# Performance work log

Measured on AMD Instinct MI355X. Metric: run time of the kernel, lower is better.

Reference implementation:

```python
import jax, jax.numpy as jnp
import numpy as np

B, N1, N2 = 4, 2048, 8192
F_IN, F_OUT = 256, 256
K = 3          # PyG knn_interpolate default
BN_EPS = 1e-5


def linear_bn(x, W, b, gamma, beta):
    # Linear + BatchNorm1d (training mode: batch stats over B*N per feature)
    h = jnp.einsum('bni,io->bno', x, W) + b
    mean = h.mean(axis=(0, 1))
    var = h.var(axis=(0, 1))
    xhat = (h - mean) * jax.lax.rsqrt(var + BN_EPS)
    return gamma * xhat + beta


def knn_interpolate(f1, p1, p2):
    # f1: [N1,F], p1: [N1,3], p2: [N2,3] -> [N2,F]
    d2 = jnp.sum((p2[:, None, :] - p1[None, :, :]) ** 2, axis=-1)  # [N2,N1]
    neg_d2, idx = jax.lax.top_k(-d2, K)                            # k smallest
    w = 1.0 / jnp.maximum(-neg_d2, 1e-16)                          # [N2,K]
    fk = f1[idx]                                                   # [N2,K,F]
    return jnp.sum(w[..., None] * fk, axis=1) / jnp.sum(w, axis=1, keepdims=True)


def setup_inputs() -> dict:
    key = jax.random.key(0)
    ks = jax.random.split(key, 10)
    return {
        'features_1': jax.random.normal(ks[0], (B, N1, F_IN), jnp.float32),
        'positions_1': jax.random.uniform(ks[1], (B, N1, 3), jnp.float32),
        'batch_1': jnp.repeat(jnp.arange(B, dtype=jnp.int64), N1),
        'features_2': jax.random.normal(ks[2], (B, N2, F_IN), jnp.float32),
        'positions_2': jax.random.uniform(ks[3], (B, N2, 3), jnp.float32),
        'batch_2': jnp.repeat(jnp.arange(B, dtype=jnp.int64), N2),
        'W1': jax.random.normal(ks[4], (F_IN, F_OUT), jnp.float32) * (1.0 / np.sqrt(F_IN)),
        'b1': jax.random.normal(ks[5], (F_OUT,), jnp.float32) * 0.02,
        'gamma1': jnp.ones((F_OUT,), jnp.float32),
        'beta1': jnp.zeros((F_OUT,), jnp.float32),
        'W2': jax.random.normal(ks[6], (F_IN, F_OUT), jnp.float32) * (1.0 / np.sqrt(F_IN)),
        'b2': jax.random.normal(ks[7], (F_OUT,), jnp.float32) * 0.02,
        'gamma2': jnp.ones((F_OUT,), jnp.float32),
        'beta2': jnp.zeros((F_OUT,), jnp.float32),
    }


def reference(features_1, positions_1, batch_1, features_2, positions_2, batch_2,
              W1, b1, gamma1, beta1, W2, b2, gamma2, beta2):
    f1 = linear_bn(features_1, W1, b1, gamma1, beta1)          # [B,N1,F_OUT]
    f2 = linear_bn(features_2, W2, b2, gamma2, beta2)          # [B,N2,F_OUT]
    # batch structure is regular [B,N]: knn restricted within batch == vmap over B
    interp = jax.vmap(knn_interpolate)(f1, positions_1, positions_2)  # [B,N2,F_OUT]
    return (interp + f2, positions_2, batch_2)
```

## Files before the change

kernel.cpp:

```cpp
#include <hip/hip_runtime.h>
#include <math.h>

#define BATCH   4
#define N1      2048
#define N2      8192
#define F       256
#define NTOT1   (BATCH * N1)
#define NTOT2   (BATCH * N2)
#define BN_EPS  1e-5f

#define GR      6
#define NC      216
#define NCP     (NC + 1)
#define GH      (1.0f / 6.0f)

typedef __attribute__((ext_vector_type(8))) short bf16x8;
typedef __attribute__((ext_vector_type(4))) float f32x4;

__device__ __forceinline__ unsigned short f2bf(float f) {
    unsigned u = __float_as_uint(f);
    unsigned r = (u + 0x7fffu + ((u >> 16) & 1u)) >> 16;
    return (unsigned short)r;
}
__device__ __forceinline__ float bflo(unsigned u) {
    return __uint_as_float(u << 16);
}
__device__ __forceinline__ float bfhi(unsigned u) {
    return __uint_as_float(u & 0xffff0000u);
}
__device__ __forceinline__ void async16(const void* g, void* l) {
    __builtin_amdgcn_global_load_lds(
        (const __attribute__((address_space(1))) unsigned int*)g,
        (__attribute__((address_space(3))) unsigned int*)l, 16, 0, 0);
}

__device__ __forceinline__ void ins3m(float d, int j,
                                      float& d0, float& d1, float& d2,
                                      int& j0, int& j1, int& j2) {
    const bool c0 = d < d0;
    const bool c1 = d < d1;
    const bool c2 = d < d2;
    const float nd1 = __builtin_amdgcn_fmed3f(d, d0, d1);
    const float nd2 = __builtin_amdgcn_fmed3f(d, d1, d2);
    d0 = fminf(d, d0);
    d1 = nd1;
    d2 = nd2;
    j2 = c1 ? j1 : (c2 ? j : j2);
    j1 = c0 ? j0 : (c1 ? j : j1);
    j0 = c0 ? j  : j0;
}

__device__ __forceinline__ int clamp6(int c) { return c < 0 ? 0 : (c > 5 ? 5 : c); }
__device__ __forceinline__ int cell_of(float x, float y, float z) {
    const int cx = clamp6((int)(x * 6.0f));
    const int cy = clamp6((int)(y * 6.0f));
    const int cz = clamp6((int)(z * 6.0f));
    return (cz * 6 + cy) * 6 + cx;
}

__global__ __launch_bounds__(256) void prep_kernel(const float4* __restrict__ f1,
                                                   const float4* __restrict__ f2,
                                                   const float* __restrict__ W1,
                                                   const float* __restrict__ W2,
                                                   const float* __restrict__ p1,
                                                   const float* __restrict__ p2,
                                                   ushort4* __restrict__ Xb1,
                                                   ushort4* __restrict__ Xb2,
                                                   unsigned short* __restrict__ Wt1,
                                                   unsigned short* __restrict__ Wt2,
                                                   float* __restrict__ sums,
                                                   float4* __restrict__ gridPts,
                                                   int* __restrict__ cellStart,
                                                   int* __restrict__ qSorted,
                                                   int* __restrict__ qCellStart) {
    const int bx = blockIdx.x;
    const int t  = threadIdx.x;

    if (bx < 8192) {
        const int i = bx * 256 + t;
        const float4 v = f2[i];
        ushort4 o;
        o.x = f2bf(v.x); o.y = f2bf(v.y); o.z = f2bf(v.z); o.w = f2bf(v.w);
        Xb2[i] = o;
    } else if (bx < 10240) {
        const int i = (bx - 8192) * 256 + t;
        const float4 v = f1[i];
        ushort4 o;
        o.x = f2bf(v.x); o.y = f2bf(v.y); o.z = f2bf(v.z); o.w = f2bf(v.w);
        Xb1[i] = o;
    } else if (bx < 10272) {
        __shared__ float tile[64][65];
        const int bb = bx - 10240;
        const bool second = bb >= 16;
        const int bl = second ? bb - 16 : bb;
        const float* W = second ? W2 : W1;
        unsigned short* Wt = second ? Wt2 : Wt1;
        const int gx0 = (bl & 3) * 64;
        const int gy0 = (bl >> 2) * 64;
        const int tx = t & 63;
        const int ty = t >> 6;
        #pragma unroll
        for (int j = 0; j < 16; ++j) {
            const int row = ty * 16 + j;
            tile[row][tx] = W[(size_t)(gy0 + row) * 256 + gx0 + tx];
        }
        __syncthreads();
        #pragma unroll
        for (int j = 0; j < 16; ++j) {
            const int row = ty * 16 + j;
            Wt[(size_t)(gx0 + row) * 256 + gy0 + tx] = f2bf(tile[tx][row]);
        }
    } else if (bx == 10272) {
        #pragma unroll
        for (int i = 0; i < 4; ++i) sums[t + 256 * i] = 0.0f;
    } else if (bx < 10277) {
        __shared__ int cnt[NC];
        __shared__ int ofs[NCP];
        const int b = bx - 10273;
        if (t < NC) cnt[t] = 0;
        __syncthreads();
        int   myc[8];
        float mx[8], my[8], mz[8];
        #pragma unroll
        for (int r = 0; r < 8; ++r) {
            const int i = r * 256 + t;
            const size_t base = (size_t)(b * N1 + i) * 3;
            mx[r] = p1[base]; my[r] = p1[base + 1]; mz[r] = p1[base + 2];
            myc[r] = cell_of(mx[r], my[r], mz[r]);
            atomicAdd(&cnt[myc[r]], 1);
        }
        __syncthreads();
        if (t <= NC) ofs[t] = (t == 0) ? 0 : cnt[t - 1];
        __syncthreads();
        for (int dd = 1; dd < NCP; dd <<= 1) {
            int v = 0;
            if (t <= NC && t >= dd) v = ofs[t - dd];
            __syncthreads();
            if (t <= NC && t >= dd) ofs[t] += v;
            __syncthreads();
        }
        if (t < NC) cnt[t] = ofs[t];
        __syncthreads();
        #pragma unroll
        for (int r = 0; r < 8; ++r) {
            const int i = r * 256 + t;
            const int pos = atomicAdd(&cnt[myc[r]], 1);
            float4 rec;
            rec.x = mx[r]; rec.y = my[r]; rec.z = mz[r];
            rec.w = __int_as_float(i);
            gridPts[(size_t)b * N1 + pos] = rec;
        }
        if (t <= NC) cellStart[b * NCP + t] = ofs[t];
    } else {
        __shared__ int cnt[NC];
        __shared__ int ofs[NCP];
        const int b = bx - 10277;
        if (t < NC) cnt[t] = 0;
        __syncthreads();
        for (int r = 0; r < 32; ++r) {
            const int i = r * 256 + t;
            const size_t base = (size_t)(b * N2 + i) * 3;
            const int c = cell_of(p2[base], p2[base + 1], p2[base + 2]);
            atomicAdd(&cnt[c], 1);
        }
        __syncthreads();
        if (t <= NC) ofs[t] = (t == 0) ? 0 : cnt[t - 1];
        __syncthreads();
        for (int dd = 1; dd < NCP; dd <<= 1) {
            int v = 0;
            if (t <= NC && t >= dd) v = ofs[t - dd];
            __syncthreads();
            if (t <= NC && t >= dd) ofs[t] += v;
            __syncthreads();
        }
        if (t < NC) cnt[t] = ofs[t];
        __syncthreads();
        for (int r = 0; r < 32; ++r) {
            const int i = r * 256 + t;
            const size_t base = (size_t)(b * N2 + i) * 3;
            const int c = cell_of(p2[base], p2[base + 1], p2[base + 2]);
            const int pos = atomicAdd(&cnt[c], 1);
            qSorted[(size_t)b * N2 + pos] = b * N2 + i;
        }
        if (t <= NC) qCellStart[b * NCP + t] = ofs[t];
    }
}

__global__ __launch_bounds__(256) void gemm_mfma_kernel(const unsigned short* __restrict__ Xb1,
                                                        const unsigned short* __restrict__ Xb2,
                                                        const unsigned short* __restrict__ Wt1,
                                                        const unsigned short* __restrict__ Wt2,
                                                        const float* __restrict__ b1,
                                                        const float* __restrict__ b2,
                                                        unsigned short* __restrict__ h1b,
                                                        unsigned short* __restrict__ h2b,
                                                        float* __restrict__ sums) {
    __shared__ unsigned short As[128 * 32];
    __shared__ unsigned short Bs[128 * 32];

    const int bx   = blockIdx.x;
    const bool g2  = bx >= 64;
    const unsigned short* Xb = g2 ? Xb2 : Xb1;
    const unsigned short* Wt = g2 ? Wt2 : Wt1;
    const float* bias        = g2 ? b2 : b1;
    unsigned short* Hb       = g2 ? h2b : h1b;
    float* sum               = sums + (g2 ? 512 : 0);
    float* sumsq             = sum + 256;
    const int row0 = (g2 ? bx - 64 : bx) * 128;
    const int n0   = blockIdx.y * 128;

    const int t    = threadIdx.x;
    const int wave = t >> 6;
    const int lane = t & 63;
    const int wm   = (wave & 1) * 64;
    const int wn   = (wave >> 1) * 64;
    const int ml   = lane & 15;
    const int q    = lane >> 4;

    f32x4 acc[4][4] = {};

    for (int kt = 0; kt < 256; kt += 32) {
        #pragma unroll
        for (int r = 0; r < 2; ++r) {
            const int e   = r * 2048 + t * 8;
            const int row = e >> 5;
            const int kk  = e & 31;
            async16(Xb + (size_t)(row0 + row) * 256 + kt + kk, (unsigned short*)As + e);
            async16(Wt + (size_t)(n0 + row) * 256 + kt + kk, (unsigned short*)Bs + e);
        }
        __syncthreads();

        bf16x8 af[4], bfr[4];
        #pragma unroll
        for (int mt = 0; mt < 4; ++mt)
            af[mt] = *(const bf16x8*)&As[(wm + mt * 16 + ml) * 32 + q * 8];
        #pragma unroll
        for (int nt = 0; nt < 4; ++nt)
            bfr[nt] = *(const bf16x8*)&Bs[(wn + nt * 16 + ml) * 32 + q * 8];
        #pragma unroll
        for (int mt = 0; mt < 4; ++mt)
            #pragma unroll
            for (int nt = 0; nt < 4; ++nt)
                acc[mt][nt] = __builtin_amdgcn_mfma_f32_16x16x32_bf16(af[mt], bfr[nt],
                                                                      acc[mt][nt], 0, 0, 0);
        __syncthreads();
    }

    float bv[4], psum[4], psq[4];
    #pragma unroll
    for (int nt = 0; nt < 4; ++nt) {
        bv[nt] = bias[n0 + wn + nt * 16 + ml];
        psum[nt] = 0.0f; psq[nt] = 0.0f;
    }
    #pragma unroll
    for (int mt = 0; mt < 4; ++mt)
        #pragma unroll
        for (int nt = 0; nt < 4; ++nt)
            #pragma unroll
            for (int r = 0; r < 4; ++r) {
                const float v = acc[mt][nt][r] + bv[nt];
                const int grow = row0 + wm + mt * 16 + q * 4 + r;
                Hb[(size_t)grow * 256 + n0 + wn + nt * 16 + ml] = f2bf(v);
                psum[nt] += v;
                psq[nt]  = fmaf(v, v, psq[nt]);
            }
    #pragma unroll
    for (int nt = 0; nt < 4; ++nt) {
        psum[nt] += __shfl_xor(psum[nt], 16, 64);
        psum[nt] += __shfl_xor(psum[nt], 32, 64);
        psq[nt]  += __shfl_xor(psq[nt], 16, 64);
        psq[nt]  += __shfl_xor(psq[nt], 32, 64);
    }
    if (q == 0) {
        #pragma unroll
        for (int nt = 0; nt < 4; ++nt) {
            const int col = n0 + wn + nt * 16 + ml;
            atomicAdd(&sum[col],   psum[nt]);
            atomicAdd(&sumsq[col], psq[nt]);
        }
    }
}

__global__ __launch_bounds__(512) void fused_kernel(const float* __restrict__ p2,
                                                    const unsigned short* __restrict__ h1b,
                                                    const unsigned short* __restrict__ h2b,
                                                    const float* __restrict__ sums,
                                                    const float* __restrict__ g1,
                                                    const float* __restrict__ be1,
                                                    const float* __restrict__ g2,
                                                    const float* __restrict__ be2,
                                                    const float4* __restrict__ gridPts,
                                                    const int* __restrict__ cellStart,
                                                    const int* __restrict__ qSorted,
                                                    const int* __restrict__ qCellStart,
                                                    float* __restrict__ out) {
    __shared__ float ssl[4][256];
    __shared__ int   cst[NCP];
    __shared__ float pdl[8][64][3];
    __shared__ int   pil[8][64][3];
    __shared__ float qdl[64][3];
    __shared__ int   qjl[64][3];
    __shared__ float wql[64][3];
    __shared__ int   jql[64][3];
    __shared__ int   qidl[64];
    __shared__ float qpx[64], qpy[64], qpz[64];

    const int t    = threadIdx.x;
    const int bx   = blockIdx.x;
    const int b    = bx / NC;
    const int cid  = bx - b * NC;
    const int ccx  = cid % 6;
    const int ccy  = (cid / 6) % 6;
    const int ccz  = cid / 36;
    const int wave = t >> 6;
    const int lane = t & 63;

    if (t < 256) {
        const float m1 = sums[t] * (1.0f / (float)NTOT1);
        const float v1 = sums[256 + t] * (1.0f / (float)NTOT1) - m1 * m1;
        const float s1 = g1[t] * rsqrtf(v1 + BN_EPS);
        ssl[0][t] = s1;
        ssl[1][t] = be1[t] - m1 * s1;
        const float m2 = sums[512 + t] * (1.0f / (float)NTOT2);
        const float v2 = sums[768 + t] * (1.0f / (float)NTOT2) - m2 * m2;
        const float s2 = g2[t] * rsqrtf(v2 + BN_EPS);
        ssl[2][t] = s2;
        ssl[3][t] = be2[t] - m2 * s2;
    }
    if (t < NCP) cst[t] = cellStart[b * NCP + t];

    const int qs = qCellStart[b * NCP + cid];
    const int qe = qCellStart[b * NCP + cid + 1];
    const float4* __restrict__ gp = gridPts + (size_t)b * N1;

    for (int q0 = qs; q0 < qe; q0 += 64) {
        const int nqc = min(64, qe - q0);
        __syncthreads();
        if (t < 64) {
            int qid = 0;
            float x = 1e30f, y = 1e30f, z = 1e30f;
            if (t < nqc) {
                qid = qSorted[(size_t)b * N2 + q0 + t];
                const size_t pb = (size_t)qid * 3;
                x = p2[pb]; y = p2[pb + 1]; z = p2[pb + 2];
            }
            qidl[t] = qid;
            qpx[t] = x; qpy[t] = y; qpz[t] = z;
        }
        __syncthreads();

        const float qx = qpx[lane], qy = qpy[lane], qz = qpz[lane];

        auto scan_box = [&](int R, float& d0, float& d1, float& d2,
                            int& i0, int& i1, int& i2) {
            const int dim  = 2 * R + 1;
            const int dim2 = dim * dim;
            const int nsl  = dim2 * dim;
            for (int sl = wave; sl < nsl; sl += 8) {
                int lz = sl / dim2;
                const int rem = sl - lz * dim2;
                int ly = rem / dim;
                int lx = rem - ly * dim;
                lx -= R; ly -= R; lz -= R;
                if (R > 1) {
                    const int ax = lx < 0 ? -lx : lx;
                    const int ay = ly < 0 ? -ly : ly;
                    const int az = lz < 0 ? -lz : lz;
                    int ch = ax > ay ? ax : ay;
                    ch = ch > az ? ch : az;
                    if (ch < R) continue;
                }
                const int gx = ccx + lx;
                const int gy = ccy + ly;
                const int gz = ccz + lz;
                if ((unsigned)gx >= 6u || (unsigned)gy >= 6u || (unsigned)gz >= 6u)
                    continue;
                const int cc = (gz * 6 + gy) * 6 + gx;
                const int s = __builtin_amdgcn_readfirstlane(cst[cc]);
                const int e = __builtin_amdgcn_readfirstlane(cst[cc + 1]);
                for (int j = s; j < e; ++j) {
                    const float4 p = gp[j];
                    const float dx = p.x - qx;
                    const float dy = p.y - qy;
                    const float dz = p.z - qz;
                    float d = dx * dx;
                    d = fmaf(dy, dy, d);
                    d = fmaf(dz, dz, d);
                    ins3m(d, __float_as_int(p.w), d0, d1, d2, i0, i1, i2);
                }
            }
        };

        auto merge_check = [&](int R) -> int {
            int notdone = 0;
            if (t < 64) {
                float m0, m1, m2;
                int a0, a1, a2;
                if (R == 1) { m0 = m1 = m2 = 1e30f; a0 = a1 = a2 = 0; }
                else {
                    m0 = qdl[t][0]; m1 = qdl[t][1]; m2 = qdl[t][2];
                    a0 = qjl[t][0]; a1 = qjl[t][1]; a2 = qjl[t][2];
                }
                #pragma unroll
                for (int s = 0; s < 8; ++s)
                    #pragma unroll
                    for (int k = 0; k < 3; ++k)
                        ins3m(pdl[s][t][k], pil[s][t][k], m0, m1, m2, a0, a1, a2);
                qdl[t][0] = m0; qdl[t][1] = m1; qdl[t][2] = m2;
                qjl[t][0] = a0; qjl[t][1] = a1; qjl[t][2] = a2;
                if (t < nqc) {
                    float dmin = 1e30f;
                    {
                        const int lo = ccx - R, hi = ccx + R;
                        if (lo > 0) dmin = fminf(dmin, qpx[t] - (float)lo * GH);
                        if (hi < 5) dmin = fminf(dmin, (float)(hi + 1) * GH - qpx[t]);
                    }
                    {
                        const int lo = ccy - R, hi = ccy + R;
                        if (lo > 0) dmin = fminf(dmin, qpy[t] - (float)lo * GH);
                        if (hi < 5) dmin = fminf(dmin, (float)(hi + 1) * GH - qpy[t]);
                    }
                    {
                        const int lo = ccz - R, hi = ccz + R;
                        if (lo > 0) dmin = fminf(dmin, qpz[t] - (float)lo * GH);
                        if (hi < 5) dmin = fminf(dmin, (float)(hi + 1) * GH - qpz[t]);
                    }
                    if (m2 > dmin * dmin * 0.9999f) notdone = 1;
                }
            }
            return __syncthreads_count(notdone);
        };

        {
            float d0 = 1e30f, d1 = 1e30f, d2 = 1e30f;
            int i0 = 0, i1 = 0, i2 = 0;
            scan_box(1, d0, d1, d2, i0, i1, i2);
            pdl[wave][lane][0] = d0; pdl[wave][lane][1] = d1; pdl[wave][lane][2] = d2;
            pil[wave][lane][0] = i0; pil[wave][lane][1] = i1; pil[wave][lane][2] = i2;
        }
        __syncthreads();
        int need = merge_check(1);
        for (int R = 2; need != 0 && R <= 6; ++R) {
            float d0 = 1e30f, d1 = 1e30f, d2 = 1e30f;
            int i0 = 0, i1 = 0, i2 = 0;
            scan_box(R, d0, d1, d2, i0, i1, i2);
            pdl[wave][lane][0] = d0; pdl[wave][lane][1] = d1; pdl[wave][lane][2] = d2;
            pil[wave][lane][0] = i0; pil[wave][lane][1] = i1; pil[wave][lane][2] = i2;
            __syncthreads();
            need = merge_check(R);
        }

        if (t < nqc) {
            const float w0 = 1.0f / fmaxf(qdl[t][0], 1e-16f);
            const float w1 = 1.0f / fmaxf(qdl[t][1], 1e-16f);
            const float w2 = 1.0f / fmaxf(qdl[t][2], 1e-16f);
            const float inv = 1.0f / (w0 + w1 + w2);
            wql[t][0] = w0 * inv; wql[t][1] = w1 * inv; wql[t][2] = w2 * inv;
            jql[t][0] = b * N1 + qjl[t][0];
            jql[t][1] = b * N1 + qjl[t][1];
            jql[t][2] = b * N1 + qjl[t][2];
        }
        __syncthreads();

        {
            const int fp = t & 127;
            const int f0 = fp * 2;
            const float s1a = ssl[0][f0],     t1a = ssl[1][f0];
            const float s2a = ssl[2][f0],     t2a = ssl[3][f0];
            const float s1b = ssl[0][f0 + 1], t1b = ssl[1][f0 + 1];
            const float s2b = ssl[2][f0 + 1], t2b = ssl[3][f0 + 1];
            for (int v = t >> 7; v < nqc; v += 4) {
                const int qid = qidl[v];
                const int   j0 = jql[v][0], j1 = jql[v][1], j2 = jql[v][2];
                const float w0 = wql[v][0], w1 = wql[v][1], w2 = wql[v][2];

                const unsigned u0 = *(const unsigned*)(h1b + (size_t)j0 * F + f0);
                const unsigned u1 = *(const unsigned*)(h1b + (size_t)j1 * F + f0);
                const unsigned u2 = *(const unsigned*)(h1b + (size_t)j2 * F + f0);
                const unsigned uh = *(const unsigned*)(h2b + (size_t)qid * F + f0);

                float alo = w0 * bflo(u0);
                alo = fmaf(w1, bflo(u1), alo);
                alo = fmaf(w2, bflo(u2), alo);
                float ahi = w0 * bfhi(u0);
                ahi = fmaf(w1, bfhi(u1), ahi);
                ahi = fmaf(w2, bfhi(u2), ahi);

                float2 o;
                o.x = fmaf(alo, s1a, t1a) + fmaf(bflo(uh), s2a, t2a);
                o.y = fmaf(ahi, s1b, t1b) + fmaf(bfhi(uh), s2b, t2b);
                *(float2*)(out + (size_t)qid * F + f0) = o;
            }
        }
    }

    if (t < 152) {
        const int tid = bx * 152 + t;
        if (tid < NTOT2 * 3) {
            out[(size_t)NTOT2 * F + tid] = p2[tid];
        } else if (tid < NTOT2 * 3 + NTOT2) {
            const int e = tid - NTOT2 * 3;
            out[(size_t)NTOT2 * F + NTOT2 * 3 + e] = (float)(e >> 13);
        }
    }
}

extern "C" void kernel_launch(void* const* d_in, const int* in_sizes, int n_in,
                              void* d_out, int out_size, void* d_ws, size_t ws_size,
                              hipStream_t stream) {
    const float* f1  = (const float*)d_in[0];
    const float* p1  = (const float*)d_in[1];
    const float* f2  = (const float*)d_in[3];
    const float* p2  = (const float*)d_in[4];
    const float* W1  = (const float*)d_in[6];
    const float* b1  = (const float*)d_in[7];
    const float* g1  = (const float*)d_in[8];
    const float* be1 = (const float*)d_in[9];
    const float* W2  = (const float*)d_in[10];
    const float* b2  = (const float*)d_in[11];
    const float* g2  = (const float*)d_in[12];
    const float* be2 = (const float*)d_in[13];

    char* ws = (char*)d_ws;
    unsigned short* Xb1   = (unsigned short*)(ws);
    unsigned short* Xb2   = (unsigned short*)(ws + 4194304);
    unsigned short* Wt1   = (unsigned short*)(ws + 20971520);
    unsigned short* Wt2   = (unsigned short*)(ws + 21102592);
    unsigned short* h1b   = (unsigned short*)(ws + 21233664);
    unsigned short* h2b   = (unsigned short*)(ws + 25427968);
    float*          sums  = (float*)(ws + 42205184);
    float4*         gridPts    = (float4*)(ws + 42209280);
    int*            cellStart  = (int*)(ws + 42340352);
    int*            qSorted    = (int*)(ws + 42343936);
    int*            qCellStart = (int*)(ws + 42475008);
    float*          out   = (float*)d_out;

    prep_kernel<<<10281, 256, 0, stream>>>((const float4*)f1, (const float4*)f2,
                                           W1, W2, p1, p2,
                                           (ushort4*)Xb1, (ushort4*)Xb2,
                                           Wt1, Wt2, sums,
                                           gridPts, cellStart, qSorted, qCellStart);

    dim3 gg(320, 2);
    gemm_mfma_kernel<<<gg, 256, 0, stream>>>(Xb1, Xb2, Wt1, Wt2, b1, b2,
                                             h1b, h2b, sums);

    fused_kernel<<<864, 512, 0, stream>>>(p2, h1b, h2b, sums,
                                          g1, be1, g2, be2,
                                          gridPts, cellStart, qSorted, qCellStart,
                                          out);
}
```

Before: 188.7 us.

## Retile GEMM to 64x64 blocks with full-K XOR-swizzled LDS staging

The BN-linear GEMM moves from 128x128 tiles with a K-loop of 32-wide chunks and two barriers per step to 64x64 tiles. Each block loads the whole K=256 slab of A and B into LDS once, using an XOR swizzle to avoid bank conflicts, then runs eight MFMA steps with no further barriers. The grid grows from 640 to 2560 blocks for better occupancy and load balance. In exchange it uses 64KB of LDS per block, does less reuse per tile (more global traffic), and issues more atomic adds for the BN statistics.

```diff
diff --git a/kernel.cpp b/kernel.cpp
--- a/kernel.cpp
+++ b/kernel.cpp
@@ -195,86 +195,87 @@
                                                         unsigned short* __restrict__ h1b,
                                                         unsigned short* __restrict__ h2b,
                                                         float* __restrict__ sums) {
-    __shared__ unsigned short As[128 * 32];
-    __shared__ unsigned short Bs[128 * 32];
+    __shared__ unsigned short As[64 * 256];
+    __shared__ unsigned short Bs[64 * 256];
 
     const int bx   = blockIdx.x;
-    const bool g2  = bx >= 64;
+    const bool g2  = bx >= 512;
     const unsigned short* Xb = g2 ? Xb2 : Xb1;
     const unsigned short* Wt = g2 ? Wt2 : Wt1;
     const float* bias        = g2 ? b2 : b1;
     unsigned short* Hb       = g2 ? h2b : h1b;
     float* sum               = sums + (g2 ? 512 : 0);
     float* sumsq             = sum + 256;
-    const int row0 = (g2 ? bx - 64 : bx) * 128;
-    const int n0   = blockIdx.y * 128;
+    const int local = g2 ? bx - 512 : bx;
+    const int mblk  = g2 ? 512 : 128;
+    const int nb    = local / mblk;
+    const int mb    = local - nb * mblk;
+    const int row0  = mb * 64;
+    const int n0    = nb * 64;
 
     const int t    = threadIdx.x;
     const int wave = t >> 6;
     const int lane = t & 63;
-    const int wm   = (wave & 1) * 64;
-    const int wn   = (wave >> 1) * 64;
+    const int wr   = wave >> 1;
+    const int wc   = wave & 1;
     const int ml   = lane & 15;
-    const int q    = lane >> 4;
-
-    f32x4 acc[4][4] = {};
-
-    for (int kt = 0; kt < 256; kt += 32) {
-        #pragma unroll
-        for (int r = 0; r < 2; ++r) {
-            const int e   = r * 2048 + t * 8;
-            const int row = e >> 5;
-            const int kk  = e & 31;
-            async16(Xb + (size_t)(row0 + row) * 256 + kt + kk, (unsigned short*)As + e);
-            async16(Wt + (size_t)(n0 + row) * 256 + kt + kk, (unsigned short*)Bs + e);
-        }
-        __syncthreads();
-
-        bf16x8 af[4], bfr[4];
-        #pragma unroll
-        for (int mt = 0; mt < 4; ++mt)
-            af[mt] = *(const bf16x8*)&As[(wm + mt * 16 + ml) * 32 + q * 8];
-        #pragma unroll
-        for (int nt = 0; nt < 4; ++nt)
-            bfr[nt] = *(const bf16x8*)&Bs[(wn + nt * 16 + ml) * 32 + q * 8];
-        #pragma unroll
-        for (int mt = 0; mt < 4; ++mt)
-            #pragma unroll
-            for (int nt = 0; nt < 4; ++nt)
-                acc[mt][nt] = __builtin_amdgcn_mfma_f32_16x16x32_bf16(af[mt], bfr[nt],
-                                                                      acc[mt][nt], 0, 0, 0);
-        __syncthreads();
-    }
-
-    float bv[4], psum[4], psq[4];
+    const int q8   = lane >> 4;
+
+    const int trow = t >> 5;
+    const int koff = ((t & 31) ^ trow) << 3;
     #pragma unroll
-    for (int nt = 0; nt < 4; ++nt) {
-        bv[nt] = bias[n0 + wn + nt * 16 + ml];
+    for (int c = 0; c < 8; ++c) {
+        async16(Xb + (size_t)(row0 + c * 8 + trow) * 256 + koff,
+                (unsigned short*)As + c * 2048 + t * 8);
+        async16(Wt + (size_t)(n0 + c * 8 + trow) * 256 + koff,
+                (unsigned short*)Bs + c * 2048 + t * 8);
+    }
+    __syncthreads();
+
+    f32x4 acc[2][2] = {};
+    const int swz = (ml & 7) << 3;
+    #pragma unroll
+    for (int ks = 0; ks < 8; ++ks) {
+        const int kz = (ks * 32 + q8 * 8) ^ swz;
+        const bf16x8 a0 = *(const bf16x8*)&As[(wr * 32 + ml) * 256 + kz];
+        const bf16x8 a1 = *(const bf16x8*)&As[(wr * 32 + 16 + ml) * 256 + kz];
+        const bf16x8 b0 = *(const bf16x8*)&Bs[(wc * 32 + ml) * 256 + kz];
+        const bf16x8 b1v = *(const bf16x8*)&Bs[(wc * 32 + 16 + ml) * 256 + kz];
+        acc[0][0] = __builtin_amdgcn_mfma_f32_16x16x32_bf16(a0, b0,  acc[0][0], 0, 0, 0);
+        acc[0][1] = __builtin_amdgcn_mfma_f32_16x16x32_bf16(a0, b1v, acc[0][1], 0, 0, 0);
+        acc[1][0] = __builtin_amdgcn_mfma_f32_16x16x32_bf16(a1, b0,  acc[1][0], 0, 0, 0);
+        acc[1][1] = __builtin_amdgcn_mfma_f32_16x16x32_bf16(a1, b1v, acc[1][1], 0, 0, 0);
+    }
+
+    float bv[2], psum[2], psq[2];
+    #pragma unroll
+    for (int nt = 0; nt < 2; ++nt) {
+        bv[nt] = bias[n0 + wc * 32 + nt * 16 + ml];
         psum[nt] = 0.0f; psq[nt] = 0.0f;
     }
     #pragma unroll
-    for (int mt = 0; mt < 4; ++mt)
-        #pragma unroll
-        for (int nt = 0; nt < 4; ++nt)
+    for (int mt = 0; mt < 2; ++mt)
+        #pragma unroll
+        for (int nt = 0; nt < 2; ++nt)
             #pragma unroll
             for (int r = 0; r < 4; ++r) {
                 const float v = acc[mt][nt][r] + bv[nt];
-                const int grow = row0 + wm + mt * 16 + q * 4 + r;
-                Hb[(size_t)grow * 256 + n0 + wn + nt * 16 + ml] = f2bf(v);
+                const int grow = row0 + wr * 32 + mt * 16 + q8 * 4 + r;
+                Hb[(size_t)grow * 256 + n0 + wc * 32 + nt * 16 + ml] = f2bf(v);
                 psum[nt] += v;
                 psq[nt]  = fmaf(v, v, psq[nt]);
             }
     #pragma unroll
-    for (int nt = 0; nt < 4; ++nt) {
+    for (int nt = 0; nt < 2; ++nt) {
         psum[nt] += __shfl_xor(psum[nt], 16, 64);
         psum[nt] += __shfl_xor(psum[nt], 32, 64);
         psq[nt]  += __shfl_xor(psq[nt], 16, 64);
         psq[nt]  += __shfl_xor(psq[nt], 32, 64);
     }
-    if (q == 0) {
-        #pragma unroll
-        for (int nt = 0; nt < 4; ++nt) {
-            const int col = n0 + wn + nt * 16 + ml;
+    if (q8 == 0) {
+        #pragma unroll
+        for (int nt = 0; nt < 2; ++nt) {
+            const int col = n0 + wc * 32 + nt * 16 + ml;
             atomicAdd(&sum[col],   psum[nt]);
             atomicAdd(&sumsq[col], psq[nt]);
         }
@@ -541,9 +542,8 @@
                                            Wt1, Wt2, sums,
                                            gridPts, cellStart, qSorted, qCellStart);
 
-    dim3 gg(320, 2);
-    gemm_mfma_kernel<<<gg, 256, 0, stream>>>(Xb1, Xb2, Wt1, Wt2, b1, b2,
-                                             h1b, h2b, sums);
+    gemm_mfma_kernel<<<2560, 256, 0, stream>>>(Xb1, Xb2, Wt1, Wt2, b1, b2,
+                                               h1b, h2b, sums);
 
     fused_kernel<<<864, 512, 0, stream>>>(p2, h1b, h2b, sums,
                                           g1, be1, g2, be2,
```

New measurement: 212.8 us. 12.8% more time.

## Fuse fp32-to-bf16 input conversion into GEMM with register-prefetched A tiles

Applied to the files above, without the earlier changes.

Removes the separate pass that converts the fp32 feature matrices to bf16 in the prep kernel. The GEMM now loads fp32 A tiles straight into registers, converts them and writes them to LDS, prefetching two k-steps ahead while B still arrives through async LDS loads. Blocks are remapped with an XCD-style interleave over a 1D grid. This saves a full write and re-read of the bf16 copies, and the prep kernel shrinks to 41 blocks. In exchange the GEMM reads twice as many A bytes, uses more registers, and now does the conversion work inside its main loop.

```diff
diff --git a/kernel.cpp b/kernel.cpp
--- a/kernel.cpp
+++ b/kernel.cpp
@@ -15,6 +15,7 @@
 #define GH      (1.0f / 6.0f)
 
 typedef __attribute__((ext_vector_type(8))) short bf16x8;
+typedef __attribute__((ext_vector_type(8))) unsigned short u16x8;
 typedef __attribute__((ext_vector_type(4))) float f32x4;
 
 __device__ __forceinline__ unsigned short f2bf(float f) {
@@ -58,14 +59,10 @@
     return (cz * 6 + cy) * 6 + cx;
 }
 
-__global__ __launch_bounds__(256) void prep_kernel(const float4* __restrict__ f1,
-                                                   const float4* __restrict__ f2,
-                                                   const float* __restrict__ W1,
+__global__ __launch_bounds__(256) void prep_kernel(const float* __restrict__ W1,
                                                    const float* __restrict__ W2,
                                                    const float* __restrict__ p1,
                                                    const float* __restrict__ p2,
-                                                   ushort4* __restrict__ Xb1,
-                                                   ushort4* __restrict__ Xb2,
                                                    unsigned short* __restrict__ Wt1,
                                                    unsigned short* __restrict__ Wt2,
                                                    float* __restrict__ sums,
@@ -76,23 +73,10 @@
     const int bx = blockIdx.x;
     const int t  = threadIdx.x;
 
-    if (bx < 8192) {
-        const int i = bx * 256 + t;
-        const float4 v = f2[i];
-        ushort4 o;
-        o.x = f2bf(v.x); o.y = f2bf(v.y); o.z = f2bf(v.z); o.w = f2bf(v.w);
-        Xb2[i] = o;
-    } else if (bx < 10240) {
-        const int i = (bx - 8192) * 256 + t;
-        const float4 v = f1[i];
-        ushort4 o;
-        o.x = f2bf(v.x); o.y = f2bf(v.y); o.z = f2bf(v.z); o.w = f2bf(v.w);
-        Xb1[i] = o;
-    } else if (bx < 10272) {
+    if (bx < 32) {
         __shared__ float tile[64][65];
-        const int bb = bx - 10240;
-        const bool second = bb >= 16;
-        const int bl = second ? bb - 16 : bb;
+        const bool second = bx >= 16;
+        const int bl = second ? bx - 16 : bx;
         const float* W = second ? W2 : W1;
         unsigned short* Wt = second ? Wt2 : Wt1;
         const int gx0 = (bl & 3) * 64;
@@ -110,13 +94,13 @@
             const int row = ty * 16 + j;
             Wt[(size_t)(gx0 + row) * 256 + gy0 + tx] = f2bf(tile[tx][row]);
         }
-    } else if (bx == 10272) {
+    } else if (bx == 32) {
         #pragma unroll
         for (int i = 0; i < 4; ++i) sums[t + 256 * i] = 0.0f;
-    } else if (bx < 10277) {
+    } else if (bx < 37) {
         __shared__ int cnt[NC];
         __shared__ int ofs[NCP];
-        const int b = bx - 10273;
+        const int b = bx - 33;
         if (t < NC) cnt[t] = 0;
         __syncthreads();
         int   myc[8];
@@ -154,7 +138,7 @@
     } else {
         __shared__ int cnt[NC];
         __shared__ int ofs[NCP];
-        const int b = bx - 10277;
+        const int b = bx - 37;
         if (t < NC) cnt[t] = 0;
         __syncthreads();
         for (int r = 0; r < 32; ++r) {
@@ -186,8 +170,8 @@
     }
 }
 
-__global__ __launch_bounds__(256) void gemm_mfma_kernel(const unsigned short* __restrict__ Xb1,
-                                                        const unsigned short* __restrict__ Xb2,
+__global__ __launch_bounds__(256) void gemm_mfma_kernel(const float* __restrict__ f1,
+                                                        const float* __restrict__ f2,
                                                         const unsigned short* __restrict__ Wt1,
                                                         const unsigned short* __restrict__ Wt2,
                                                         const float* __restrict__ b1,
@@ -198,16 +182,21 @@
     __shared__ unsigned short As[128 * 32];
     __shared__ unsigned short Bs[128 * 32];
 
-    const int bx   = blockIdx.x;
-    const bool g2  = bx >= 64;
-    const unsigned short* Xb = g2 ? Xb2 : Xb1;
+    const int bx = blockIdx.x;
+    const int L  = (bx & 7) * 80 + (bx >> 3);
+    const bool g2 = L >= 128;
+    const int ll  = g2 ? L - 128 : L;
+    const int mb  = ll >> 1;
+    const int nbi = ll & 1;
+
+    const float* Fsrc        = g2 ? f2 : f1;
     const unsigned short* Wt = g2 ? Wt2 : Wt1;
     const float* bias        = g2 ? b2 : b1;
     unsigned short* Hb       = g2 ? h2b : h1b;
     float* sum               = sums + (g2 ? 512 : 0);
     float* sumsq             = sum + 256;
-    const int row0 = (g2 ? bx - 64 : bx) * 128;
-    const int n0   = blockIdx.y * 128;
+    const int row0 = mb * 128;
+    const int n0   = nbi * 128;
 
     const int t    = threadIdx.x;
     const int wave = t >> 6;
@@ -217,19 +206,53 @@
     const int ml   = lane & 15;
     const int q    = lane >> 4;
 
-    f32x4 acc[4][4] = {};
-
-    for (int kt = 0; kt < 256; kt += 32) {
+    float4 arA[2], arB[2];
+    auto loadA = [&](int kt) {
+        #pragma unroll
+        for (int i = 0; i < 2; ++i) {
+            const int pi  = i * 256 + t;
+            const int row = pi >> 2;
+            const int q2  = pi & 3;
+            const float4* src = (const float4*)Fsrc
+                              + (size_t)(row0 + row) * 64 + kt * 8 + q2 * 2;
+            arA[i] = src[0];
+            arB[i] = src[1];
+        }
+    };
+    auto writeA = [&]() {
+        #pragma unroll
+        for (int i = 0; i < 2; ++i) {
+            const int pi  = i * 256 + t;
+            const int row = pi >> 2;
+            const int q2  = pi & 3;
+            u16x8 v;
+            v[0] = f2bf(arA[i].x); v[1] = f2bf(arA[i].y);
+            v[2] = f2bf(arA[i].z); v[3] = f2bf(arA[i].w);
+            v[4] = f2bf(arB[i].x); v[5] = f2bf(arB[i].y);
+            v[6] = f2bf(arB[i].z); v[7] = f2bf(arB[i].w);
+            *(u16x8*)&As[row * 32 + q2 * 8] = v;
+        }
+    };
+    auto stageB = [&](int kt) {
         #pragma unroll
         for (int r = 0; r < 2; ++r) {
             const int e   = r * 2048 + t * 8;
             const int row = e >> 5;
             const int kk  = e & 31;
-            async16(Xb + (size_t)(row0 + row) * 256 + kt + kk, (unsigned short*)As + e);
-            async16(Wt + (size_t)(n0 + row) * 256 + kt + kk, (unsigned short*)Bs + e);
-        }
-        __syncthreads();
-
+            async16(Wt + (size_t)(n0 + row) * 256 + kt * 32 + kk,
+                    (unsigned short*)Bs + e);
+        }
+    };
+
+    f32x4 acc[4][4] = {};
+
+    loadA(0);
+    stageB(0);
+    writeA();
+    loadA(1);
+    __syncthreads();
+
+    for (int kt = 0; kt < 8; ++kt) {
         bf16x8 af[4], bfr[4];
         #pragma unroll
         for (int mt = 0; mt < 4; ++mt)
@@ -243,7 +266,13 @@
             for (int nt = 0; nt < 4; ++nt)
                 acc[mt][nt] = __builtin_amdgcn_mfma_f32_16x16x32_bf16(af[mt], bfr[nt],
                                                                       acc[mt][nt], 0, 0, 0);
-        __syncthreads();
+        if (kt < 7) {
+            __syncthreads();
+            stageB(kt + 1);
+            writeA();
+            if (kt < 6) loadA(kt + 2);
+            __syncthreads();
+        }
     }
 
     float bv[4], psum[4], psq[4];
@@ -522,28 +551,23 @@
     const float* be2 = (const float*)d_in[13];
 
     char* ws = (char*)d_ws;
-    unsigned short* Xb1   = (unsigned short*)(ws);
-    unsigned short* Xb2   = (unsigned short*)(ws + 4194304);
-    unsigned short* Wt1   = (unsigned short*)(ws + 20971520);
-    unsigned short* Wt2   = (unsigned short*)(ws + 21102592);
-    unsigned short* h1b   = (unsigned short*)(ws + 21233664);
-    unsigned short* h2b   = (unsigned short*)(ws + 25427968);
-    float*          sums  = (float*)(ws + 42205184);
-    float4*         gridPts    = (float4*)(ws + 42209280);
-    int*            cellStart  = (int*)(ws + 42340352);
-    int*            qSorted    = (int*)(ws + 42343936);
-    int*            qCellStart = (int*)(ws + 42475008);
+    unsigned short* Wt1   = (unsigned short*)(ws);
+    unsigned short* Wt2   = (unsigned short*)(ws + 131072);
+    unsigned short* h1b   = (unsigned short*)(ws + 262144);
+    unsigned short* h2b   = (unsigned short*)(ws + 4456448);
+    float*          sums  = (float*)(ws + 21233664);
+    float4*         gridPts    = (float4*)(ws + 21237760);
+    int*            cellStart  = (int*)(ws + 21368832);
+    int*            qSorted    = (int*)(ws + 21372416);
+    int*            qCellStart = (int*)(ws + 21503488);
     float*          out   = (float*)d_out;
 
-    prep_kernel<<<10281, 256, 0, stream>>>((const float4*)f1, (const float4*)f2,
-                                           W1, W2, p1, p2,
-                                           (ushort4*)Xb1, (ushort4*)Xb2,
-                                           Wt1, Wt2, sums,
-                                           gridPts, cellStart, qSorted, qCellStart);
-
-    dim3 gg(320, 2);
-    gemm_mfma_kernel<<<gg, 256, 0, stream>>>(Xb1, Xb2, Wt1, Wt2, b1, b2,
-                                             h1b, h2b, sums);
+    prep_kernel<<<41, 256, 0, stream>>>(W1, W2, p1, p2,
+                                        Wt1, Wt2, sums,
+                                        gridPts, cellStart, qSorted, qCellStart);
+
+    gemm_mfma_kernel<<<640, 256, 0, stream>>>(f1, f2, Wt1, Wt2, b1, b2,
+                                              h1b, h2b, sums);
 
     fused_kernel<<<864, 512, 0, stream>>>(p2, h1b, h2b, sums,
                                           g1, be1, g2, be2,
```

Result: faster. 181.2 us (-4.0%).
